# Optimization experiments

Hardware: AMD Instinct MI355X
Metric: run time of the kernel (lower is better)

Reference implementation:

```python
import jax, jax.numpy as jnp
import numpy as np

N_NODES = 200_000  # total nodes (segment id space for the CSR-style grouped reduce)


def setup_inputs() -> dict:
    key = jax.random.key(0)
    k1, k2, k3, k4, k5 = jax.random.split(key, 5)
    E, D = 1_000_000, 128   # interaction events, message dim
    B, K = 50_000, 20       # neighbor-attention batch, neighbors per node
    node_ids = jax.random.randint(k1, (E,), 0, N_NODES, dtype=jnp.int64)
    message = jax.random.normal(k2, (E, D), dtype=jnp.float32)
    timestamps = jax.random.uniform(k3, (E, 1), dtype=jnp.float32)
    nei1 = jax.random.normal(k4, (B, K, D), dtype=jnp.float32)
    nei2 = jax.random.normal(k5, (B, K, D), dtype=jnp.float32)
    return {"node_ids": node_ids, "message": message, "timestamps": timestamps,
            "nei1": nei1, "nei2": nei2}


def reference(node_ids, message, timestamps, nei1, nei2):
    # --- merged_by_segment_csr: grouped reduction over variable-length event groups.
    # torch does sort + unique_consecutive + cumsum + segment_csr; in jax the
    # equivalent (and efficient) form is a fixed-size segment reduce keyed by node id.
    ones = jnp.ones((node_ids.shape[0],), dtype=message.dtype)
    counts = jax.ops.segment_sum(ones, node_ids, num_segments=N_NODES)          # [N]
    msg_sum = jax.ops.segment_sum(message, node_ids, num_segments=N_NODES)      # [N, D]
    # msg_agg == 'mean' (segment_csr mean); empty segments yield 0.
    merged_message = msg_sum / jnp.maximum(counts, 1.0)[:, None]
    merged_t = jax.ops.segment_max(timestamps, node_ids, num_segments=N_NODES)  # [N, 1]
    merged_t = jnp.where(counts[:, None] > 0, merged_t, jnp.zeros_like(merged_t))
    # --- NeighborAttention: matmul(node1, node2^T).sum(dim=2) -> softmax over dim 0.
    # sum_j (n1[k] . n2[j]) == n1[k] . sum_j n2[j]  (avoids the [B,K,K] intermediate)
    logits = jnp.einsum('bkd,bd->bk', nei1, nei2.sum(axis=1))                   # [B, K]
    score = jax.nn.softmax(logits, axis=0)  # softmax over dim=0, as in the module
    return (merged_message, merged_t, score)
```

## Files before the change

kernel.cpp:

```cpp
#include <hip/hip_runtime.h>

#define N_NODES 200000
#define E_EVENTS 1000000
#define D_DIM 128
#define B_BATCH 50000
#define K_NEI 20

#define SCAN_BLK 196


__global__ void hist(const int* __restrict__ ids, int* __restrict__ counts)
{
    int e = blockIdx.x * blockDim.x + threadIdx.x;
    if (e < E_EVENTS) atomicAdd(counts + ids[e], 1);
}

__global__ void scan_block(const int* __restrict__ counts, int* __restrict__ blockSums)
{
    __shared__ int sd[256];
    int t = threadIdx.x, base = blockIdx.x * 1024 + t * 4;
    int s = 0;
#pragma unroll
    for (int j = 0; j < 4; ++j) { int i = base + j; if (i < N_NODES) s += counts[i]; }
    sd[t] = s; __syncthreads();
    for (int off = 128; off; off >>= 1) {
        if (t < off) sd[t] += sd[t + off];
        __syncthreads();
    }
    if (t == 0) blockSums[blockIdx.x] = sd[0];
}

__global__ void scan_tops(int* __restrict__ blockSums)
{
    __shared__ int sd[256];
    int t = threadIdx.x;
    int v = (t < SCAN_BLK) ? blockSums[t] : 0;
    sd[t] = v; __syncthreads();
    for (int off = 1; off < 256; off <<= 1) {
        int x = (t >= off) ? sd[t - off] : 0;
        __syncthreads();
        sd[t] += x;
        __syncthreads();
    }
    if (t < SCAN_BLK) blockSums[t] = sd[t] - v;
}

__global__ void scan_final(const int* __restrict__ counts, const int* __restrict__ blockSums,
                           int* __restrict__ offsets, int* __restrict__ cursor)
{
    __shared__ int sd[256];
    int t = threadIdx.x, base = blockIdx.x * 1024 + t * 4;
    int c[4];
#pragma unroll
    for (int j = 0; j < 4; ++j) { int i = base + j; c[j] = (i < N_NODES) ? counts[i] : 0; }
    int tsum = c[0] + c[1] + c[2] + c[3];
    sd[t] = tsum; __syncthreads();
    for (int off = 1; off < 256; off <<= 1) {
        int x = (t >= off) ? sd[t - off] : 0;
        __syncthreads();
        sd[t] += x;
        __syncthreads();
    }
    int excl = sd[t] - tsum + blockSums[blockIdx.x];
#pragma unroll
    for (int j = 0; j < 4; ++j) {
        int i = base + j;
        if (i < N_NODES) { offsets[i] = excl; cursor[i] = excl; }
        excl += c[j];
    }
}

__global__ void scatter(const int* __restrict__ ids, int* __restrict__ cursor,
                        int* __restrict__ perm)
{
    int e = blockIdx.x * blockDim.x + threadIdx.x;
    if (e < E_EVENTS) {
        int pos = atomicAdd(cursor + ids[e], 1);
        perm[pos] = e;
    }
}

__global__ void __launch_bounds__(256, 8)
seg_attn(const int* __restrict__ perm, const int* __restrict__ offsets,
         const int* __restrict__ counts,
         const float* __restrict__ message, const float* __restrict__ ts,
         const float* __restrict__ nei1, const float* __restrict__ nei2,
         float* __restrict__ msg_out, float* __restrict__ t_out,
         float* __restrict__ logits)
{
    int g = blockIdx.x / 5, r = blockIdx.x % 5;
    int wid  = threadIdx.x >> 6;
    int lane = threadIdx.x & 63;

    if (r < 4) {
        int n = (g * 4 + r) * 4 + wid;
        int start = offsets[n];
        int len   = counts[n];
        const float2* msg2 = reinterpret_cast<const float2*>(message);
        float2 a0 = make_float2(0.f, 0.f), a1 = make_float2(0.f, 0.f);
        float tmax = 0.f;
        for (int base = 0; base < len; base += 64) {
            int cl = min(len - base, 64);
            int   e_l = 0;
            float t_l = 0.f;
            if (lane < cl) {
                e_l = perm[start + base + lane];
                t_l = ts[e_l];
            }
            tmax = fmaxf(tmax, t_l);
            int i = 0;
            for (; i + 4 <= cl; i += 4) {
                int e0 = __shfl(e_l, i);
                int e1 = __shfl(e_l, i + 1);
                int e2 = __shfl(e_l, i + 2);
                int e3 = __shfl(e_l, i + 3);
                float2 m0 = msg2[(size_t)e0 * 64 + lane];
                float2 m1 = msg2[(size_t)e1 * 64 + lane];
                float2 m2 = msg2[(size_t)e2 * 64 + lane];
                float2 m3 = msg2[(size_t)e3 * 64 + lane];
                a0.x += m0.x; a0.y += m0.y;
                a1.x += m1.x; a1.y += m1.y;
                a0.x += m2.x; a0.y += m2.y;
                a1.x += m3.x; a1.y += m3.y;
            }
            for (; i < cl; ++i) {
                int e = __shfl(e_l, i);
                float2 m = msg2[(size_t)e * 64 + lane];
                a0.x += m.x; a0.y += m.y;
            }
        }
        float inv = 1.0f / (float)max(len, 1);
        float2 acc = make_float2((a0.x + a1.x) * inv, (a0.y + a1.y) * inv);
        reinterpret_cast<float2*>(msg_out)[(size_t)n * 64 + lane] = acc;
#pragma unroll
        for (int off = 32; off; off >>= 1) tmax = fmaxf(tmax, __shfl_xor(tmax, off));
        if (lane == 0) t_out[n] = tmax;
    } else {
        int b = g * 4 + wid;
        int d4   = lane & 31;
        int half = lane >> 5;
        const float4* n2 = reinterpret_cast<const float4*>(nei2) + (size_t)b * (K_NEI * 32);
        float4 acc = make_float4(0.f, 0.f, 0.f, 0.f);
#pragma unroll
        for (int i = 0; i < K_NEI / 2; ++i) {
            float4 v = n2[(2 * i + half) * 32 + d4];
            acc.x += v.x; acc.y += v.y; acc.z += v.z; acc.w += v.w;
        }
        float4 s4;
        s4.x = acc.x + __shfl_xor(acc.x, 32);
        s4.y = acc.y + __shfl_xor(acc.y, 32);
        s4.z = acc.z + __shfl_xor(acc.z, 32);
        s4.w = acc.w + __shfl_xor(acc.w, 32);

        const float4* n1 = reinterpret_cast<const float4*>(nei1) + (size_t)b * (K_NEI * 32);
#pragma unroll
        for (int i = 0; i < K_NEI / 2; ++i) {
            int k = 2 * i + half;
            float4 v = n1[k * 32 + d4];
            float p = v.x * s4.x + v.y * s4.y + v.z * s4.z + v.w * s4.w;
#pragma unroll
            for (int off = 16; off; off >>= 1) p += __shfl_xor(p, off);
            if (d4 == 0) logits[(size_t)b * K_NEI + k] = p;
        }
    }
}

__global__ void softmax_partial(const float* __restrict__ logits, float2* __restrict__ partials)
{
    int t = threadIdx.x;
    float m[K_NEI], s[K_NEI];
#pragma unroll
    for (int k = 0; k < K_NEI; ++k) { m[k] = -INFINITY; s[k] = 0.f; }

    for (int b = blockIdx.x * 256 + t; b < B_BATCH; b += 128 * 256) {
        const float4* row = reinterpret_cast<const float4*>(logits + (size_t)b * K_NEI);
        float v[K_NEI];
#pragma unroll
        for (int q = 0; q < 5; ++q) {
            float4 rr = row[q];
            v[q * 4 + 0] = rr.x; v[q * 4 + 1] = rr.y; v[q * 4 + 2] = rr.z; v[q * 4 + 3] = rr.w;
        }
#pragma unroll
        for (int k = 0; k < K_NEI; ++k) {
            float nm = fmaxf(m[k], v[k]);
            s[k] = s[k] * expf(m[k] - nm) + expf(v[k] - nm);
            m[k] = nm;
        }
    }
#pragma unroll
    for (int k = 0; k < K_NEI; ++k) {
#pragma unroll
        for (int off = 32; off; off >>= 1) {
            float om = __shfl_xor(m[k], off);
            float os = __shfl_xor(s[k], off);
            float nm = fmaxf(m[k], om);
            s[k] = s[k] * expf(m[k] - nm) + os * expf(om - nm);
            m[k] = nm;
        }
    }
    __shared__ float lm[4][K_NEI], lsum[4][K_NEI];
    int wid = t >> 6, lane = t & 63;
    if (lane == 0) {
#pragma unroll
        for (int k = 0; k < K_NEI; ++k) { lm[wid][k] = m[k]; lsum[wid][k] = s[k]; }
    }
    __syncthreads();
    if (t < K_NEI) {
        float mm = lm[0][t], ss = lsum[0][t];
#pragma unroll
        for (int w = 1; w < 4; ++w) {
            float om = lm[w][t], os = lsum[w][t];
            float nm = fmaxf(mm, om);
            ss = ss * expf(mm - nm) + os * expf(om - nm);
            mm = nm;
        }
        partials[blockIdx.x * K_NEI + t] = make_float2(mm, ss);
    }
}

__global__ void softmax_final(const float2* __restrict__ partials, float2* __restrict__ stats)
{
    int t = threadIdx.x;
    if (t < K_NEI) {
        float mm = -INFINITY, ss = 0.f;
        for (int i = 0; i < 128; ++i) {
            float2 p = partials[i * K_NEI + t];
            float nm = fmaxf(mm, p.x);
            ss = ss * expf(mm - nm) + p.y * expf(p.x - nm);
            mm = nm;
        }
        stats[t] = make_float2(mm, ss);
    }
}

__global__ void softmax_norm(float* __restrict__ score, const float2* __restrict__ stats)
{
    int i = blockIdx.x * blockDim.x + threadIdx.x;
    if (i >= B_BATCH * K_NEI) return;
    int k = i % K_NEI;
    float2 st = stats[k];
    score[i] = expf(score[i] - st.x) / st.y;
}

extern "C" void kernel_launch(void* const* d_in, const int* in_sizes, int n_in,
                              void* d_out, int out_size, void* d_ws, size_t ws_size,
                              hipStream_t stream)
{
    const int*   node_ids = (const int*)  d_in[0];
    const float* message  = (const float*)d_in[1];
    const float* ts       = (const float*)d_in[2];
    const float* nei1     = (const float*)d_in[3];
    const float* nei2     = (const float*)d_in[4];

    float* out     = (float*)d_out;
    float* msg_out = out;
    float* t_out   = out + (size_t)N_NODES * D_DIM;
    float* score   = t_out + N_NODES;

    int*    wsi       = (int*)d_ws;
    int*    counts    = wsi;
    int*    offsets   = wsi + 200000;
    int*    cursor    = wsi + 400000;
    int*    blockSums = wsi + 600000;
    int*    perm      = wsi + 600320;
    float2* stats     = (float2*)(wsi + 1600320);
    float2* partials  = (float2*)(wsi + 1600384);

    hipMemsetAsync(counts, 0, (size_t)N_NODES * sizeof(int), stream);

    hist<<<(E_EVENTS + 255) / 256, 256, 0, stream>>>(node_ids, counts);
    scan_block<<<SCAN_BLK, 256, 0, stream>>>(counts, blockSums);
    scan_tops<<<1, 256, 0, stream>>>(blockSums);
    scan_final<<<SCAN_BLK, 256, 0, stream>>>(counts, blockSums, offsets, cursor);
    scatter<<<(E_EVENTS + 255) / 256, 256, 0, stream>>>(node_ids, cursor, perm);

    seg_attn<<<12500 * 5, 256, 0, stream>>>(
        perm, offsets, counts, message, ts, nei1, nei2, msg_out, t_out, score);

    softmax_partial<<<128, 256, 0, stream>>>(score, partials);
    softmax_final<<<1, 64, 0, stream>>>(partials, stats);
    softmax_norm<<<(B_BATCH * K_NEI + 255) / 256, 256, 0, stream>>>(score, stats);
}
```

Measured before the change: 476.3 us.

## Process 13 consecutive segments per wave with a flattened event stream

Each wave in the segment-reduce branch now handles 13 consecutive nodes and walks their combined CSR event range in one stream. When it crosses a segment boundary it flushes the mean and max for that node. Event loads are batched 8 at a time to raise memory-level parallelism and to stop waves from idling on short segments, which average about 5 events each. The grid is reshaped to 4 segment blocks and 13 attention blocks per group, which changes the ratio of segment work to attention work. The per-element boundary check and the extra branching add divergence-free scalar overhead, and ts is now also shuffled per element.

```diff
diff --git a/kernel.cpp b/kernel.cpp
--- a/kernel.cpp
+++ b/kernel.cpp
@@ -7,6 +7,11 @@
 #define K_NEI 20
 
 #define SCAN_BLK 196
+#define NODES_PER_WAVE 13
+#define SEG_WAVES ((N_NODES + NODES_PER_WAVE - 1) / NODES_PER_WAVE)
+#define SEG_BLOCKS ((SEG_WAVES + 3) / 4)
+#define ATTN_BLOCKS (B_BATCH / 4)
+#define N_GROUPS 962
 
 
 __global__ void hist(const int* __restrict__ ids, int* __restrict__ counts)
@@ -82,61 +87,83 @@
 
 __global__ void __launch_bounds__(256, 8)
 seg_attn(const int* __restrict__ perm, const int* __restrict__ offsets,
-         const int* __restrict__ counts,
          const float* __restrict__ message, const float* __restrict__ ts,
          const float* __restrict__ nei1, const float* __restrict__ nei2,
          float* __restrict__ msg_out, float* __restrict__ t_out,
          float* __restrict__ logits)
 {
-    int g = blockIdx.x / 5, r = blockIdx.x % 5;
+    int g = blockIdx.x / 17, r = blockIdx.x % 17;
     int wid  = threadIdx.x >> 6;
     int lane = threadIdx.x & 63;
 
     if (r < 4) {
-        int n = (g * 4 + r) * 4 + wid;
-        int start = offsets[n];
-        int len   = counts[n];
+        int wwid = (g * 4 + r) * 4 + wid;
+        int n0 = wwid * NODES_PER_WAVE;
+        if (n0 >= N_NODES) return;
+        int nl = min(NODES_PER_WAVE, N_NODES - n0);
+        int bnd = E_EVENTS;
+        if (lane <= nl && n0 + lane < N_NODES) bnd = offsets[n0 + lane];
+        int start = __shfl(bnd, 0);
+        int end   = __shfl(bnd, nl);
+
         const float2* msg2 = reinterpret_cast<const float2*>(message);
-        float2 a0 = make_float2(0.f, 0.f), a1 = make_float2(0.f, 0.f);
+        float2* out2 = reinterpret_cast<float2*>(msg_out);
+
+        float2 acc = make_float2(0.f, 0.f);
         float tmax = 0.f;
-        for (int base = 0; base < len; base += 64) {
-            int cl = min(len - base, 64);
-            int   e_l = 0;
-            float t_l = 0.f;
+        int node = 0;
+        int nb = __shfl(bnd, 1);
+
+        for (int base = start; base < end; base += 64) {
+            int cl = min(end - base, 64);
+            int e_l = 0; float t_l = 0.f;
             if (lane < cl) {
-                e_l = perm[start + base + lane];
+                e_l = perm[base + lane];
                 t_l = ts[e_l];
             }
-            tmax = fmaxf(tmax, t_l);
-            int i = 0;
-            for (; i + 4 <= cl; i += 4) {
-                int e0 = __shfl(e_l, i);
-                int e1 = __shfl(e_l, i + 1);
-                int e2 = __shfl(e_l, i + 2);
-                int e3 = __shfl(e_l, i + 3);
-                float2 m0 = msg2[(size_t)e0 * 64 + lane];
-                float2 m1 = msg2[(size_t)e1 * 64 + lane];
-                float2 m2 = msg2[(size_t)e2 * 64 + lane];
-                float2 m3 = msg2[(size_t)e3 * 64 + lane];
-                a0.x += m0.x; a0.y += m0.y;
-                a1.x += m1.x; a1.y += m1.y;
-                a0.x += m2.x; a0.y += m2.y;
-                a1.x += m3.x; a1.y += m3.y;
+            for (int i0 = 0; i0 < 64; i0 += 8) {
+                if (i0 >= cl) break;
+                float2 rr[8]; float tt[8];
+#pragma unroll
+                for (int j = 0; j < 8; ++j) {
+                    int idx = i0 + j; if (idx >= cl) idx = cl - 1;
+                    int e  = __shfl(e_l, idx);
+                    tt[j]  = __shfl(t_l, idx);
+                    rr[j]  = msg2[(size_t)e * 64 + lane];
+                }
+#pragma unroll
+                for (int j = 0; j < 8; ++j) {
+                    if (i0 + j < cl) {
+                        int i = base + i0 + j;
+                        while (i == nb) {
+                            int lo = __shfl(bnd, node), hi = nb;
+                            float inv = 1.0f / (float)max(hi - lo, 1);
+                            out2[(size_t)(n0 + node) * 64 + lane] =
+                                make_float2(acc.x * inv, acc.y * inv);
+                            if (lane == 0) t_out[n0 + node] = tmax;
+                            acc = make_float2(0.f, 0.f); tmax = 0.f;
+                            ++node;
+                            nb = __shfl(bnd, node + 1);
+                        }
+                        acc.x += rr[j].x; acc.y += rr[j].y;
+                        tmax = fmaxf(tmax, tt[j]);
+                    }
+                }
             }
-            for (; i < cl; ++i) {
-                int e = __shfl(e_l, i);
-                float2 m = msg2[(size_t)e * 64 + lane];
-                a0.x += m.x; a0.y += m.y;
-            }
-        }
-        float inv = 1.0f / (float)max(len, 1);
-        float2 acc = make_float2((a0.x + a1.x) * inv, (a0.y + a1.y) * inv);
-        reinterpret_cast<float2*>(msg_out)[(size_t)n * 64 + lane] = acc;
-#pragma unroll
-        for (int off = 32; off; off >>= 1) tmax = fmaxf(tmax, __shfl_xor(tmax, off));
-        if (lane == 0) t_out[n] = tmax;
+        }
+        while (node < nl) {
+            int lo = __shfl(bnd, node), hi = __shfl(bnd, node + 1);
+            float inv = 1.0f / (float)max(hi - lo, 1);
+            out2[(size_t)(n0 + node) * 64 + lane] =
+                make_float2(acc.x * inv, acc.y * inv);
+            if (lane == 0) t_out[n0 + node] = tmax;
+            acc = make_float2(0.f, 0.f); tmax = 0.f;
+            ++node;
+        }
     } else {
-        int b = g * 4 + wid;
+        int ab = g * 13 + (r - 4);
+        if (ab >= ATTN_BLOCKS) return;
+        int b = ab * 4 + wid;
         int d4   = lane & 31;
         int half = lane >> 5;
         const float4* n2 = reinterpret_cast<const float4*>(nei2) + (size_t)b * (K_NEI * 32);
@@ -274,8 +301,8 @@
     scan_final<<<SCAN_BLK, 256, 0, stream>>>(counts, blockSums, offsets, cursor);
     scatter<<<(E_EVENTS + 255) / 256, 256, 0, stream>>>(node_ids, cursor, perm);
 
-    seg_attn<<<12500 * 5, 256, 0, stream>>>(
-        perm, offsets, counts, message, ts, nei1, nei2, msg_out, t_out, score);
+    seg_attn<<<N_GROUPS * 17, 256, 0, stream>>>(
+        perm, offsets, message, ts, nei1, nei2, msg_out, t_out, score);
 
     softmax_partial<<<128, 256, 0, stream>>>(score, partials);
     softmax_final<<<1, 64, 0, stream>>>(partials, stats);
```

After: 505.4 us. 1.06x slower.

## Pack timestamps into permutation and widen segment gather to float4 half-waves

Applied to the files above, without the earlier changes.

The scatter kernel can now write (event, timestamp) pairs into the permutation, so the segment kernel no longer does a dependent random load of the timestamp. Which path runs depends on the workspace size. The message gather switches from float2 per lane to float4 loads, with each half-wave covering a different event, and the halves are combined by a shuffle at the end. Segment length now comes from adjacent offsets instead of the counts array. The logits write is also coalesced into one 20-lane store per row. In exchange, the permutation takes twice the workspace, and when the workspace is too small the code falls back to the old timestamp load.

```diff
diff --git a/kernel.cpp b/kernel.cpp
--- a/kernel.cpp
+++ b/kernel.cpp
@@ -70,80 +70,105 @@
     }
 }
 
-__global__ void scatter(const int* __restrict__ ids, int* __restrict__ cursor,
-                        int* __restrict__ perm)
+template<int TSP>
+__global__ void scatter_t(const int* __restrict__ ids, const float* __restrict__ ts,
+                          int* __restrict__ cursor, void* __restrict__ permv)
 {
     int e = blockIdx.x * blockDim.x + threadIdx.x;
     if (e < E_EVENTS) {
         int pos = atomicAdd(cursor + ids[e], 1);
-        perm[pos] = e;
-    }
-}
-
+        if (TSP) ((int2*)permv)[pos] = make_int2(e, __float_as_int(ts[e]));
+        else     ((int*)permv)[pos]  = e;
+    }
+}
+
+template<int TSP>
 __global__ void __launch_bounds__(256, 8)
-seg_attn(const int* __restrict__ perm, const int* __restrict__ offsets,
-         const int* __restrict__ counts,
-         const float* __restrict__ message, const float* __restrict__ ts,
-         const float* __restrict__ nei1, const float* __restrict__ nei2,
-         float* __restrict__ msg_out, float* __restrict__ t_out,
-         float* __restrict__ logits)
+seg_attn_t(const void* __restrict__ permv, const int* __restrict__ offsets,
+           const float* __restrict__ message, const float* __restrict__ ts,
+           const float* __restrict__ nei1, const float* __restrict__ nei2,
+           float* __restrict__ msg_out, float* __restrict__ t_out,
+           float* __restrict__ logits)
 {
     int g = blockIdx.x / 5, r = blockIdx.x % 5;
     int wid  = threadIdx.x >> 6;
     int lane = threadIdx.x & 63;
+    int c = lane & 31;
+    int h = lane >> 5;
 
     if (r < 4) {
         int n = (g * 4 + r) * 4 + wid;
         int start = offsets[n];
-        int len   = counts[n];
-        const float2* msg2 = reinterpret_cast<const float2*>(message);
-        float2 a0 = make_float2(0.f, 0.f), a1 = make_float2(0.f, 0.f);
+        int end   = (n < N_NODES - 1) ? offsets[n + 1] : E_EVENTS;
+        int len   = end - start;
+
+        const float4* msg4 = reinterpret_cast<const float4*>(message);
+        float4 acc0 = make_float4(0.f, 0.f, 0.f, 0.f);
+        float4 acc1 = make_float4(0.f, 0.f, 0.f, 0.f);
         float tmax = 0.f;
-        for (int base = 0; base < len; base += 64) {
-            int cl = min(len - base, 64);
-            int   e_l = 0;
-            float t_l = 0.f;
+
+        for (int base = start; base < end; base += 64) {
+            int cl = min(end - base, 64);
+            int e_l = 0; float t_l = 0.f;
             if (lane < cl) {
-                e_l = perm[start + base + lane];
-                t_l = ts[e_l];
+                if (TSP) {
+                    int2 pe = ((const int2*)permv)[base + lane];
+                    e_l = pe.x; t_l = __int_as_float(pe.y);
+                } else {
+                    e_l = ((const int*)permv)[base + lane];
+                    t_l = ts[e_l];
+                }
             }
             tmax = fmaxf(tmax, t_l);
             int i = 0;
-            for (; i + 4 <= cl; i += 4) {
-                int e0 = __shfl(e_l, i);
-                int e1 = __shfl(e_l, i + 1);
-                int e2 = __shfl(e_l, i + 2);
-                int e3 = __shfl(e_l, i + 3);
-                float2 m0 = msg2[(size_t)e0 * 64 + lane];
-                float2 m1 = msg2[(size_t)e1 * 64 + lane];
-                float2 m2 = msg2[(size_t)e2 * 64 + lane];
-                float2 m3 = msg2[(size_t)e3 * 64 + lane];
-                a0.x += m0.x; a0.y += m0.y;
-                a1.x += m1.x; a1.y += m1.y;
-                a0.x += m2.x; a0.y += m2.y;
-                a1.x += m3.x; a1.y += m3.y;
+            for (; i + 8 <= cl; i += 8) {
+                int eA = __shfl(e_l, i + 0 + h);
+                int eB = __shfl(e_l, i + 2 + h);
+                int eC = __shfl(e_l, i + 4 + h);
+                int eD = __shfl(e_l, i + 6 + h);
+                float4 vA = msg4[(size_t)eA * 32 + c];
+                float4 vB = msg4[(size_t)eB * 32 + c];
+                float4 vC = msg4[(size_t)eC * 32 + c];
+                float4 vD = msg4[(size_t)eD * 32 + c];
+                acc0.x += vA.x; acc0.y += vA.y; acc0.z += vA.z; acc0.w += vA.w;
+                acc1.x += vB.x; acc1.y += vB.y; acc1.z += vB.z; acc1.w += vB.w;
+                acc0.x += vC.x; acc0.y += vC.y; acc0.z += vC.z; acc0.w += vC.w;
+                acc1.x += vD.x; acc1.y += vD.y; acc1.z += vD.z; acc1.w += vD.w;
             }
-            for (; i < cl; ++i) {
+            for (; i + 2 <= cl; i += 2) {
+                int e = __shfl(e_l, i + h);
+                float4 v = msg4[(size_t)e * 32 + c];
+                acc0.x += v.x; acc0.y += v.y; acc0.z += v.z; acc0.w += v.w;
+            }
+            if (i < cl) {
                 int e = __shfl(e_l, i);
-                float2 m = msg2[(size_t)e * 64 + lane];
-                a0.x += m.x; a0.y += m.y;
+                if (h == 0) {
+                    float4 v = msg4[(size_t)e * 32 + c];
+                    acc0.x += v.x; acc0.y += v.y; acc0.z += v.z; acc0.w += v.w;
+                }
             }
         }
+        float4 acc = make_float4(acc0.x + acc1.x, acc0.y + acc1.y,
+                                 acc0.z + acc1.z, acc0.w + acc1.w);
+        acc.x += __shfl_xor(acc.x, 32);
+        acc.y += __shfl_xor(acc.y, 32);
+        acc.z += __shfl_xor(acc.z, 32);
+        acc.w += __shfl_xor(acc.w, 32);
         float inv = 1.0f / (float)max(len, 1);
-        float2 acc = make_float2((a0.x + a1.x) * inv, (a0.y + a1.y) * inv);
-        reinterpret_cast<float2*>(msg_out)[(size_t)n * 64 + lane] = acc;
+        if (h == 0) {
+            reinterpret_cast<float4*>(msg_out)[(size_t)n * 32 + c] =
+                make_float4(acc.x * inv, acc.y * inv, acc.z * inv, acc.w * inv);
+        }
 #pragma unroll
         for (int off = 32; off; off >>= 1) tmax = fmaxf(tmax, __shfl_xor(tmax, off));
         if (lane == 0) t_out[n] = tmax;
     } else {
         int b = g * 4 + wid;
-        int d4   = lane & 31;
-        int half = lane >> 5;
         const float4* n2 = reinterpret_cast<const float4*>(nei2) + (size_t)b * (K_NEI * 32);
         float4 acc = make_float4(0.f, 0.f, 0.f, 0.f);
 #pragma unroll
         for (int i = 0; i < K_NEI / 2; ++i) {
-            float4 v = n2[(2 * i + half) * 32 + d4];
+            float4 v = n2[(2 * i + h) * 32 + c];
             acc.x += v.x; acc.y += v.y; acc.z += v.z; acc.w += v.w;
         }
         float4 s4;
@@ -153,15 +178,21 @@
         s4.w = acc.w + __shfl_xor(acc.w, 32);
 
         const float4* n1 = reinterpret_cast<const float4*>(nei1) + (size_t)b * (K_NEI * 32);
+        float p[K_NEI / 2];
 #pragma unroll
         for (int i = 0; i < K_NEI / 2; ++i) {
-            int k = 2 * i + half;
-            float4 v = n1[k * 32 + d4];
-            float p = v.x * s4.x + v.y * s4.y + v.z * s4.z + v.w * s4.w;
-#pragma unroll
-            for (int off = 16; off; off >>= 1) p += __shfl_xor(p, off);
-            if (d4 == 0) logits[(size_t)b * K_NEI + k] = p;
-        }
+            float4 v = n1[(2 * i + h) * 32 + c];
+            float pp = v.x * s4.x + v.y * s4.y + v.z * s4.z + v.w * s4.w;
+#pragma unroll
+            for (int off = 16; off; off >>= 1) pp += __shfl_xor(pp, off);
+            p[i] = pp;
+        }
+        int sel = c >> 1;
+        float v = p[0];
+#pragma unroll
+        for (int i = 1; i < K_NEI / 2; ++i) v = (sel == i) ? p[i] : v;
+        float vf = __shfl(v, ((lane & 1) << 5) + c);
+        if (lane < K_NEI) logits[(size_t)b * K_NEI + lane] = vf;
     }
 }
 
@@ -262,9 +293,11 @@
     int*    offsets   = wsi + 200000;
     int*    cursor    = wsi + 400000;
     int*    blockSums = wsi + 600000;
-    int*    perm      = wsi + 600320;
-    float2* stats     = (float2*)(wsi + 1600320);
-    float2* partials  = (float2*)(wsi + 1600384);
+    float2* stats     = (float2*)(wsi + 600256);
+    float2* partials  = (float2*)(wsi + 600320);
+    void*   permv     = (void*)(wsi + 605440);
+
+    bool tsp = ws_size >= ((size_t)605440 * 4 + (size_t)E_EVENTS * 8);
 
     hipMemsetAsync(counts, 0, (size_t)N_NODES * sizeof(int), stream);
 
@@ -272,10 +305,16 @@
     scan_block<<<SCAN_BLK, 256, 0, stream>>>(counts, blockSums);
     scan_tops<<<1, 256, 0, stream>>>(blockSums);
     scan_final<<<SCAN_BLK, 256, 0, stream>>>(counts, blockSums, offsets, cursor);
-    scatter<<<(E_EVENTS + 255) / 256, 256, 0, stream>>>(node_ids, cursor, perm);
-
-    seg_attn<<<12500 * 5, 256, 0, stream>>>(
-        perm, offsets, counts, message, ts, nei1, nei2, msg_out, t_out, score);
+
+    if (tsp) {
+        scatter_t<1><<<(E_EVENTS + 255) / 256, 256, 0, stream>>>(node_ids, ts, cursor, permv);
+        seg_attn_t<1><<<12500 * 5, 256, 0, stream>>>(
+            permv, offsets, message, ts, nei1, nei2, msg_out, t_out, score);
+    } else {
+        scatter_t<0><<<(E_EVENTS + 255) / 256, 256, 0, stream>>>(node_ids, ts, cursor, permv);
+        seg_attn_t<0><<<12500 * 5, 256, 0, stream>>>(
+            permv, offsets, message, ts, nei1, nei2, msg_out, t_out, score);
+    }
 
     softmax_partial<<<128, 256, 0, stream>>>(score, partials);
     softmax_final<<<1, 64, 0, stream>>>(partials, stats);
```

Result: no change. 472.4 us (-0.8%).
